# Kernel tuning notes

Measured on AMD Instinct MI355X. Metric: run time of the kernel, lower is better.

Reference implementation:

```python
import jax, jax.numpy as jnp
import numpy as np

C, S, K, SIGMA = 512, 11, 3, 16
B = 128
EPS = 1e-5  # BatchNorm eps (eval mode, running_mean=0, running_var=1)


def _make_dct_weight(Cc, H, W):
    # FcaNet 'low16' frequency selection
    lx = [0, 0, 1, 1, 0, 2, 2, 1, 2, 0, 3, 4, 0, 1, 3, 0]
    ly = [0, 1, 0, 1, 2, 0, 1, 2, 2, 3, 0, 0, 4, 3, 1, 5]
    mx = [u * (H // 7) for u in lx]
    my = [v * (W // 7) for v in ly]
    w = np.zeros((Cc, H, W), np.float32)
    cp = Cc // len(lx)

    def bf(pos, freq, POS):
        r = np.cos(np.pi * freq * (pos + 0.5) / POS) / np.sqrt(POS)
        return r if freq == 0 else r * np.sqrt(2.0)

    for i, (u, v) in enumerate(zip(mx, my)):
        for tx in range(H):
            for ty in range(W):
                w[i * cp:(i + 1) * cp, tx, ty] = bf(tx, u, H) * bf(ty, v, W)
    return jnp.asarray(w)


def _bn(f, g, b):
    # eval-mode BatchNorm2d: (f - 0)/sqrt(1+eps)*g + b, per channel (axis 1)
    s = g / jnp.sqrt(1.0 + EPS)
    return f * s[None, :, None, None] + b[None, :, None, None]


def _conv1x1(f, w, b):
    return jnp.einsum('bchw,oc->bohw', f, w) + b[None, :, None, None]


def _spatial_kernel(f, w_conv, b_conv, g_sp, b_sp):
    Bn = f.shape[0]
    s = _conv1x1(f, w_conv, b_conv)                  # (B, K*K, S, S)
    s = s.reshape(Bn, K * K, S * S).transpose(0, 2, 1)  # (B, S*S, K*K)
    s = _bn(s.reshape(Bn, S * S, K, K), g_sp, b_sp)
    return s.reshape(Bn, S * S, K * K)


def _channel_kernel(f, dct_w, fc1, fc2, g_ch, b_ch):
    y = jnp.sum(f * dct_w[None], axis=(-2, -1))      # (B, C) DCT pooling
    y = jax.nn.sigmoid(jax.nn.relu(y @ fc1.T) @ fc2.T)  # (B, C*K*K)
    y = _bn(y.reshape(-1, C, K, K), g_ch, b_ch)
    return y.reshape(-1, C, K * K)


def _unfold(f):
    # torch-style per-pixel kxk neighborhoods -> (B, C, H, W, K, K)
    p = (K + 1) // 2 - 1
    Bn, Cn, H, W = f.shape
    fp = jnp.pad(f, ((0, 0), (0, 0), (p, p), (p, p)))
    pat = jnp.stack([fp[:, :, di:di + H, dj:dj + W]
                     for di in range(K) for dj in range(K)], axis=-1)
    return pat.reshape(Bn, Cn, H, W, K, K)


def setup_inputs() -> dict:
    key = jax.random.key(0)
    ks = iter(jax.random.split(key, 32))

    def nrm(shape, s=0.02):
        return s * jax.random.normal(next(ks), shape, jnp.float32)

    def gma(shape):
        return 1.0 + 0.1 * jax.random.normal(next(ks), shape, jnp.float32)

    return dict(
        x=jax.random.normal(next(ks), (B, C, S, S), jnp.float32),
        dct_w=_make_dct_weight(C, S, S),
        w_conv=nrm((K * K, C)), b_conv=nrm((K * K,)),
        g_sp=gma((S * S,)), b_sp=nrm((S * S,), 0.05),
        g_ch=gma((C,)), b_ch=nrm((C,), 0.05),
        fc1=nrm((C // SIGMA, C)), fc2=nrm((C * K * K, C // SIGMA)),
        up_w1=nrm((2 * C, C)), up_b1=nrm((2 * C,)), up_g1=gma((2 * C,)), up_bb1=nrm((2 * C,), 0.05),
        up_w2=nrm((2 * C, 2 * C)), up_b2=nrm((2 * C,)), up_g2=gma((2 * C,)), up_bb2=nrm((2 * C,), 0.05),
        lo_w1=nrm((2 * C, 2 * C)), lo_b1=nrm((2 * C,)), lo_g1=gma((2 * C,)), lo_bb1=nrm((2 * C,), 0.05),
        lo_w2=nrm((C, 2 * C)), lo_b2=nrm((C,)), lo_g2=gma((C,)), lo_bb2=nrm((C,), 0.05),
    )


def reference(x, dct_w, w_conv, b_conv, g_sp, b_sp, g_ch, b_ch, fc1, fc2,
              up_w1, up_b1, up_g1, up_bb1, up_w2, up_b2, up_g2, up_bb2,
              lo_w1, lo_b1, lo_g1, lo_bb1, lo_w2, lo_b2, lo_g2, lo_bb2):
    Bn = x.shape[0]
    # instance kernel: spatial (B,1,HW,KK) x channel (B,C,1,KK)
    sk = _spatial_kernel(x, w_conv, b_conv, g_sp, b_sp)[:, None]
    ck = _channel_kernel(x, dct_w, fc1, fc2, g_ch, b_ch)[:, :, None]
    inst = (sk * ck).reshape(Bn, C, S, S, K, K)
    # CLM task representation (sum over batch between upper and lower)
    a = jax.nn.relu(_bn(_conv1x1(x, up_w1, up_b1), up_g1, up_bb1))
    a = jax.nn.relu(_bn(_conv1x1(a, up_w2, up_b2), up_g2, up_bb2))
    a = a.sum(axis=0, keepdims=True)
    a = jax.nn.relu(_bn(_conv1x1(a, lo_w1, lo_b1), lo_g1, lo_bb1))
    task_s = jax.nn.sigmoid(_bn(_conv1x1(a, lo_w2, lo_b2), lo_g2, lo_bb2))
    # task kernel (shared across the batch)
    sk_t = _spatial_kernel(task_s, w_conv, b_conv, g_sp, b_sp)[:, None]
    ck_t = _channel_kernel(task_s, dct_w, fc1, fc2, g_ch, b_ch)[:, :, None]
    task_kernel = (sk_t * ck_t).reshape(1, C, S, S, K, K)
    kernel = task_kernel * inst
    adapted = (_unfold(x) * kernel).mean(axis=(-1, -2))  # (B,C,S,S)
    return adapted + x, task_kernel
```

## Files before the change

kernel.cpp:

```cpp
#include <hip/hip_runtime.h>
#include <hip/hip_bf16.h>
#include <math.h>

#define BNEPS 1e-5f
#define BDIM_B 128
#define CDIM 512
#define SS 121
#define KK 9
#define MROWS (BDIM_B * SS)

typedef unsigned short u16;
typedef __bf16 bf16x8 __attribute__((ext_vector_type(8)));
typedef float f32x4 __attribute__((ext_vector_type(4)));

__device__ __forceinline__ u16 f2bf(float f) {
    union { float f; unsigned int u; } v; v.f = f;
    unsigned int r = v.u + 0x7FFF + ((v.u >> 16) & 1);
    return (u16)(r >> 16);
}
__device__ __forceinline__ float bf2f(u16 v) {
    union { unsigned int u; float f; } x; x.u = ((unsigned int)v) << 16; return x.f;
}

__device__ __forceinline__ void gld16(const u16* g, u16* l) {
    __builtin_amdgcn_global_load_lds(
        (const __attribute__((address_space(1))) void*)g,
        (__attribute__((address_space(3))) void*)l, 16, 0, 0);
}

template<int MODE>
__global__ __launch_bounds__(256)
void gemm_mfma(const u16* __restrict__ A, const u16* __restrict__ Bw,
               const float* __restrict__ bias, const float* __restrict__ g,
               const float* __restrict__ bb, void* __restrict__ out, int Kd)
{
    __shared__ __align__(16) u16 Als[128 * 32];
    __shared__ __align__(16) u16 Bls[128 * 32];

    const int tid  = threadIdx.x;
    const int lane = tid & 63;
    const int w    = tid >> 6;
    const int wm   = w >> 1, wn = w & 1;
    const int bm   = blockIdx.x * 128;
    const int bn   = blockIdx.y * 128;

    f32x4 acc[4][4] = {};

    const int subrow = tid >> 2;
    const int kq     = tid & 3;
    const u16* Ab = A  + (size_t)(bm + subrow) * Kd + kq * 8;
    const u16* Bb = Bw + (size_t)(bn + subrow) * Kd + kq * 8;
    u16* Al0 = &Als[(w * 16) * 32];
    u16* Al1 = &Als[(w * 16 + 64) * 32];
    u16* Bl0 = &Bls[(w * 16) * 32];
    u16* Bl1 = &Bls[(w * 16 + 64) * 32];

    const int fa_row = wm * 64 + (lane & 15);
    const int fb_row = wn * 64 + (lane & 15);
    const int kofs   = (lane >> 4) * 8;

    for (int k0 = 0; k0 < Kd; k0 += 32) {
        __syncthreads();
        gld16(Ab + k0, Al0);
        gld16(Ab + (size_t)64 * Kd + k0, Al1);
        gld16(Bb + k0, Bl0);
        gld16(Bb + (size_t)64 * Kd + k0, Bl1);
        __syncthreads();

        bf16x8 af[4], bfv[4];
        #pragma unroll
        for (int i = 0; i < 4; ++i)
            af[i] = *(bf16x8*)&Als[(fa_row + i * 16) * 32 + kofs];
        #pragma unroll
        for (int j = 0; j < 4; ++j)
            bfv[j] = *(bf16x8*)&Bls[(fb_row + j * 16) * 32 + kofs];
        #pragma unroll
        for (int i = 0; i < 4; ++i)
            #pragma unroll
            for (int j = 0; j < 4; ++j)
                acc[i][j] = __builtin_amdgcn_mfma_f32_16x16x32_bf16(af[i], bfv[j], acc[i][j], 0, 0, 0);
    }

    const float inv = 1.0f / sqrtf(1.0f + BNEPS);

    if (MODE == 1) {
        u16* Y = (u16*)out;
        int dstrow[4][4];
        #pragma unroll
        for (int i = 0; i < 4; ++i) {
            int mb = bm + wm * 64 + i * 16 + (lane >> 4) * 4;
            #pragma unroll
            for (int r = 0; r < 4; ++r) {
                int m = mb + r;
                int b = m / 121, p = m - b * 121;
                dstrow[i][r] = p * 128 + b;
            }
        }
        #pragma unroll
        for (int j = 0; j < 4; ++j) {
            int n = bn + wn * 64 + j * 16 + (lane & 15);
            float sc = g[n] * inv, bo = bias[n], bv = bb[n];
            #pragma unroll
            for (int i = 0; i < 4; ++i)
                #pragma unroll
                for (int r = 0; r < 4; ++r) {
                    float v = (acc[i][j][r] + bo) * sc + bv;
                    v = fmaxf(v, 0.0f);
                    Y[(size_t)dstrow[i][r] * 1024 + n] = f2bf(v);
                }
        }
    } else {
        float ps[4];
        #pragma unroll
        for (int j = 0; j < 4; ++j) {
            int n = bn + wn * 64 + j * 16 + (lane & 15);
            float sc = g[n] * inv, bo = bias[n], bv = bb[n];
            float s = 0.f;
            #pragma unroll
            for (int i = 0; i < 4; ++i)
                #pragma unroll
                for (int r = 0; r < 4; ++r) {
                    float v = (acc[i][j][r] + bo) * sc + bv;
                    s += fmaxf(v, 0.0f);
                }
            ps[j] = s;
        }
        __syncthreads();
        float* red = (float*)Als;
        #pragma unroll
        for (int j = 0; j < 4; ++j)
            red[(wm * 4 + (lane >> 4)) * 128 + wn * 64 + j * 16 + (lane & 15)] = ps[j];
        __syncthreads();
        if (tid < 128) {
            float s = 0.f;
            #pragma unroll
            for (int r = 0; r < 8; ++r) s += red[r * 128 + tid];
            ((float*)out)[(size_t)blockIdx.x * 1024 + bn + tid] = s;
        }
    }
}

__global__ void transpose_x(const float* __restrict__ x, u16* __restrict__ Xb)
{
    __shared__ float t[64 * 121];
    int b = blockIdx.x, c0 = blockIdx.y * 64;
    for (int idx = threadIdx.x; idx < 64 * 121; idx += 256) {
        int c = idx / 121, p = idx - c * 121;
        t[idx] = x[((size_t)b * 512 + c0 + c) * 121 + p];
    }
    __syncthreads();
    for (int idx = threadIdx.x; idx < 121 * 64; idx += 256) {
        int p = idx >> 6, c = idx & 63;
        Xb[((size_t)(b * 121 + p)) * 512 + c0 + c] = f2bf(t[c * 121 + p]);
    }
}

__global__ void f32_to_bf16(const float* __restrict__ in, u16* __restrict__ out, int n)
{
    int i = blockIdx.x * 256 + threadIdx.x;
    if (i < n) out[i] = f2bf(in[i]);
}

__global__ void transpose_dct(const float* __restrict__ dct, float* __restrict__ dctT)
{
    int idx = blockIdx.x * 256 + threadIdx.x;
    if (idx >= 512 * 121) return;
    int p = idx >> 9, c = idx & 511;
    dctT[idx] = dct[(size_t)c * 121 + p];
}

template<int ACT>
__global__ __launch_bounds__(256)
void fc_ksplit(const float* __restrict__ A, const float* __restrict__ W,
               const float* __restrict__ bias, const float* __restrict__ g,
               const float* __restrict__ bb, void* __restrict__ out,
               int N, int Kd)
{
    __shared__ float Als[1024];
    int p = blockIdx.x;
    const float* a = A + (size_t)p * Kd;
    for (int i = threadIdx.x; i < Kd / 4; i += 256)
        ((float4*)Als)[i] = ((const float4*)a)[i];
    __syncthreads();
    int n = blockIdx.y * 64 + (threadIdx.x >> 2);
    int kp = threadIdx.x & 3;
    const float* w = W + (size_t)n * Kd;
    float s0 = 0.f, s1 = 0.f;
    for (int k = kp * 4; k < Kd; k += 32) {
        float4 wv = *(const float4*)(w + k);
        float4 av = *(const float4*)(Als + k);
        s0 += wv.x * av.x + wv.y * av.y + wv.z * av.z + wv.w * av.w;
        float4 wv2 = *(const float4*)(w + k + 16);
        float4 av2 = *(const float4*)(Als + k + 16);
        s1 += wv2.x * av2.x + wv2.y * av2.y + wv2.z * av2.z + wv2.w * av2.w;
    }
    float s = s0 + s1;
    s += __shfl_xor(s, 1);
    s += __shfl_xor(s, 2);
    if (kp == 0) {
        s = (s + bias[n]) * (g[n] * (1.0f / sqrtf(1.0f + BNEPS))) + bb[n];
        if (ACT == 0) {
            ((float*)out)[(size_t)p * N + n] = fmaxf(s, 0.f);
        } else {
            s = 1.f / (1.f + expf(-s));
            ((u16*)out)[(size_t)p * 512 + n] = f2bf(s);
        }
    }
}

__global__ __launch_bounds__(256)
void rowdot9(const u16* __restrict__ Xb, const u16* __restrict__ Xt,
             const float* __restrict__ w_conv, const float* __restrict__ b_conv,
             const float* __restrict__ g_sp, const float* __restrict__ b_sp,
             float* __restrict__ skb, float* __restrict__ skt)
{
    int wid = (blockIdx.x * 256 + threadIdx.x) >> 6;
    int lane = threadIdx.x & 63;
    if (wid >= MROWS + SS) return;
    const u16* src = (wid < MROWS) ? Xb + (size_t)wid * 512
                                   : Xt + (size_t)(wid - MROWS) * 512;
    bf16x8 xv = *(const bf16x8*)(src + lane * 8);
    float xf[8];
    #pragma unroll
    for (int j = 0; j < 8; ++j) xf[j] = (float)xv[j];

    float s[9];
    #pragma unroll
    for (int k9 = 0; k9 < 9; ++k9) {
        const float* wr = w_conv + k9 * 512 + lane * 8;
        float4 w0 = *(const float4*)wr;
        float4 w1 = *(const float4*)(wr + 4);
        s[k9] = xf[0] * w0.x + xf[1] * w0.y + xf[2] * w0.z + xf[3] * w0.w
              + xf[4] * w1.x + xf[5] * w1.y + xf[6] * w1.z + xf[7] * w1.w;
    }
    #pragma unroll
    for (int off = 1; off < 64; off <<= 1)
        #pragma unroll
        for (int k9 = 0; k9 < 9; ++k9)
            s[k9] += __shfl_xor(s[k9], off);

    if (lane < 9) {
        int p = wid % 121;
        float v = (s[lane] + b_conv[lane]) * (g_sp[p] * (1.0f / sqrtf(1.0f + BNEPS))) + b_sp[p];
        float* dst = (wid < MROWS) ? skb + (size_t)wid * 9 : skt + (size_t)(wid - MROWS) * 9;
        dst[lane] = v;
    }
}

__global__ void dct_pool_xb(const u16* __restrict__ Xb, const u16* __restrict__ Xt,
                            const float* __restrict__ dctT,
                            float* __restrict__ ybuf, float* __restrict__ y_t)
{
    int idx = blockIdx.x * 256 + threadIdx.x;
    if (idx >= 129 * 512) return;
    int g = idx >> 9, c = idx & 511;
    const u16* src = (g < 128) ? Xb + (size_t)g * 121 * 512 + c : Xt + c;
    float s = 0.f;
    for (int p = 0; p < SS; ++p)
        s += bf2f(src[(size_t)p * 512]) * dctT[p * 512 + c];
    if (g < 128) ybuf[idx] = s; else y_t[c] = s;
}

__global__ __launch_bounds__(256)
void fc1_fused(const float* __restrict__ ybuf, const float* __restrict__ y_t,
               const float* __restrict__ fc1, float* __restrict__ y2buf,
               float* __restrict__ y2_t)
{
    __shared__ float Als[512];
    int g = blockIdx.x;
    const float* a = (g < 128) ? ybuf + (size_t)g * 512 : y_t;
    for (int i = threadIdx.x; i < 128; i += 256)
        ((float4*)Als)[i] = ((const float4*)a)[i];
    __syncthreads();
    int o = threadIdx.x >> 3, kp = threadIdx.x & 7;
    const float* w = fc1 + (size_t)o * 512;
    float s = 0.f;
    for (int k = kp * 4; k < 512; k += 32) {
        float4 wv = *(const float4*)(w + k);
        float4 av = *(const float4*)(Als + k);
        s += wv.x * av.x + wv.y * av.y + wv.z * av.z + wv.w * av.w;
    }
    s += __shfl_xor(s, 1);
    s += __shfl_xor(s, 2);
    s += __shfl_xor(s, 4);
    if (kp == 0) {
        float v = fmaxf(s, 0.f);
        if (g < 128) y2buf[(size_t)g * 32 + o] = v; else y2_t[o] = v;
    }
}

__global__ void fc2_ck_fused(const float* __restrict__ y2buf, const float* __restrict__ y2_t,
                             const float* __restrict__ fc2,
                             const float* __restrict__ g_ch, const float* __restrict__ b_ch,
                             float* __restrict__ ckbuf, float* __restrict__ ck_t)
{
    int idx = blockIdx.x * 256 + threadIdx.x;
    if (idx >= 129 * CDIM * KK) return;
    int g = idx / (CDIM * KK), o = idx % (CDIM * KK);
    int c = o / KK;
    const float* yb = (g < 128) ? y2buf + (size_t)g * 32 : y2_t;
    const float* w = fc2 + (size_t)o * 32;
    float s = 0.f;
    #pragma unroll
    for (int k = 0; k < 32; ++k) s += yb[k] * w[k];
    s = 1.f / (1.f + expf(-s));
    s = s * (g_ch[c] * (1.0f / sqrtf(1.0f + BNEPS))) + b_ch[c];
    if (g < 128) ckbuf[idx] = s; else ck_t[o] = s;
}

__global__ void task_kernel_write(const float* __restrict__ sk_t, const float* __restrict__ ck_t,
                                  float* __restrict__ tk)
{
    int idx = blockIdx.x * blockDim.x + threadIdx.x;
    if (idx >= CDIM * SS * KK) return;
    int k9 = idx % KK;
    int pc = idx / KK;
    int p = pc % SS, c = pc / SS;
    tk[idx] = sk_t[p * KK + k9] * ck_t[c * KK + k9];
}

__global__ __launch_bounds__(256)
void final_v2(const float* __restrict__ x, const float* __restrict__ skb,
              const float* __restrict__ sk_t, const float* __restrict__ ckbuf,
              const float* __restrict__ ck_t, float* __restrict__ out0)
{
    __shared__ float PS[SS * KK];
    __shared__ float CS[64 * KK];
    __shared__ float XT[64 * SS];
    const int tid = threadIdx.x;
    const int b = blockIdx.x, c0 = blockIdx.y * 64;

    const float* sp = skb + (size_t)b * SS * KK;
    for (int i = tid; i < SS * KK; i += 256) PS[i] = sp[i] * sk_t[i];
    const float* cp = ckbuf + ((size_t)b * CDIM + c0) * KK;
    const float* tp = ck_t + (size_t)c0 * KK;
    for (int i = tid; i < 64 * KK; i += 256) CS[i] = cp[i] * tp[i];
    const float* xp = x + ((size_t)b * CDIM + c0) * SS;
    for (int i = tid; i < 64 * SS; i += 256) XT[i] = xp[i];
    __syncthreads();

    float* op = out0 + ((size_t)b * CDIM + c0) * SS;
    for (int i = tid; i < 64 * SS; i += 256) {
        int c = i / SS, p = i - c * SS;
        int h = p / 11, w = p - h * 11;
        const float* xc = XT + c * SS;
        const float* ps = PS + p * KK;
        const float* cs = CS + c * KK;
        float acc = 0.f;
        #pragma unroll
        for (int di = 0; di < 3; ++di) {
            int hh = h + di - 1;
            bool hv = (unsigned)hh < 11u;
            #pragma unroll
            for (int dj = 0; dj < 3; ++dj) {
                int ww = w + dj - 1;
                int k = di * 3 + dj;
                float xv = (hv && (unsigned)ww < 11u) ? xc[hh * 11 + ww] : 0.f;
                acc += xv * ps[k] * cs[k];
            }
        }
        op[i] = acc * (1.0f / 9.0f) + xc[p];
    }
}

extern "C" void kernel_launch(void* const* d_in, const int* in_sizes, int n_in,
                              void* d_out, int out_size, void* d_ws, size_t ws_size,
                              hipStream_t stream)
{
    const float* x      = (const float*)d_in[0];
    const float* dct_w  = (const float*)d_in[1];
    const float* w_conv = (const float*)d_in[2];
    const float* b_conv = (const float*)d_in[3];
    const float* g_sp   = (const float*)d_in[4];
    const float* b_sp   = (const float*)d_in[5];
    const float* g_ch   = (const float*)d_in[6];
    const float* b_ch   = (const float*)d_in[7];
    const float* fc1    = (const float*)d_in[8];
    const float* fc2    = (const float*)d_in[9];
    const float* up_w1  = (const float*)d_in[10];
    const float* up_b1  = (const float*)d_in[11];
    const float* up_g1  = (const float*)d_in[12];
    const float* up_bb1 = (const float*)d_in[13];
    const float* up_w2  = (const float*)d_in[14];
    const float* up_b2  = (const float*)d_in[15];
    const float* up_g2  = (const float*)d_in[16];
    const float* up_bb2 = (const float*)d_in[17];
    const float* lo_w1  = (const float*)d_in[18];
    const float* lo_b1  = (const float*)d_in[19];
    const float* lo_g1  = (const float*)d_in[20];
    const float* lo_bb1 = (const float*)d_in[21];
    const float* lo_w2  = (const float*)d_in[22];
    const float* lo_b2  = (const float*)d_in[23];
    const float* lo_g2  = (const float*)d_in[24];
    const float* lo_bb2 = (const float*)d_in[25];

    float* out0 = (float*)d_out;
    float* tk   = out0 + (size_t)BDIM_B * CDIM * SS;

    char* ws = (char*)d_ws;
    size_t off = 0;
    auto alloc = [&](size_t bytes) { void* p = ws + off; off += (bytes + 63) & ~(size_t)63; return p; };
    u16*   Xb     = (u16*)alloc((size_t)MROWS * 512 * 2);
    u16*   Y1     = (u16*)alloc((size_t)MROWS * 1024 * 2);
    u16*   w1b    = (u16*)alloc((size_t)1024 * 512 * 2);
    u16*   w2b    = (u16*)alloc((size_t)1024 * 1024 * 2);
    float* asum   = (float*)alloc((size_t)SS * 1024 * 4);
    float* a3     = (float*)alloc((size_t)SS * 1024 * 4);
    u16*   ts_pc  = (u16*)alloc((size_t)SS * 512 * 2);
    float* dctT   = (float*)alloc((size_t)SS * 512 * 4);
    float* ybuf   = (float*)alloc((size_t)BDIM_B * CDIM * 4);
    float* y2buf  = (float*)alloc((size_t)BDIM_B * 32 * 4);
    float* ckbuf  = (float*)alloc((size_t)BDIM_B * CDIM * KK * 4);
    float* skbuf  = (float*)alloc((size_t)BDIM_B * SS * KK * 4);
    float* y_t    = (float*)alloc((size_t)CDIM * 4);
    float* y2_t   = (float*)alloc((size_t)32 * 4);
    float* ck_t   = (float*)alloc((size_t)CDIM * KK * 4);
    float* sk_t   = (float*)alloc((size_t)SS * KK * 4);

    hipLaunchKernelGGL(transpose_x, dim3(BDIM_B, 8), dim3(256), 0, stream, x, Xb);
    hipLaunchKernelGGL(f32_to_bf16, dim3((1024 * 512 + 255) / 256), dim3(256), 0, stream,
                       up_w1, w1b, 1024 * 512);
    hipLaunchKernelGGL(f32_to_bf16, dim3((1024 * 1024 + 255) / 256), dim3(256), 0, stream,
                       up_w2, w2b, 1024 * 1024);
    hipLaunchKernelGGL(transpose_dct, dim3((512 * 121 + 255) / 256), dim3(256), 0, stream,
                       dct_w, dctT);

    dim3 ggrid(MROWS / 128, 1024 / 128);
    hipLaunchKernelGGL((gemm_mfma<1>), ggrid, dim3(256), 0, stream,
                       Xb, w1b, up_b1, up_g1, up_bb1, (void*)Y1, 512);
    hipLaunchKernelGGL((gemm_mfma<2>), ggrid, dim3(256), 0, stream,
                       Y1, w2b, up_b2, up_g2, up_bb2, (void*)asum, 1024);

    hipLaunchKernelGGL((fc_ksplit<0>), dim3(SS, 16), dim3(256), 0, stream,
                       asum, lo_w1, lo_b1, lo_g1, lo_bb1, (void*)a3, 1024, 1024);
    hipLaunchKernelGGL((fc_ksplit<1>), dim3(SS, 8), dim3(256), 0, stream,
                       a3, lo_w2, lo_b2, lo_g2, lo_bb2, (void*)ts_pc, 512, 1024);

    hipLaunchKernelGGL(rowdot9, dim3((MROWS + SS + 3) / 4), dim3(256), 0, stream,
                       Xb, ts_pc, w_conv, b_conv, g_sp, b_sp, skbuf, sk_t);

    hipLaunchKernelGGL(dct_pool_xb, dim3((129 * 512) / 256), dim3(256), 0, stream,
                       Xb, ts_pc, dctT, ybuf, y_t);
    hipLaunchKernelGGL(fc1_fused, dim3(129), dim3(256), 0, stream,
                       ybuf, y_t, fc1, y2buf, y2_t);
    hipLaunchKernelGGL(fc2_ck_fused, dim3((129 * CDIM * KK + 255) / 256), dim3(256), 0, stream,
                       y2buf, y2_t, fc2, g_ch, b_ch, ckbuf, ck_t);

    hipLaunchKernelGGL(task_kernel_write, dim3((CDIM * SS * KK + 255) / 256), dim3(256), 0, stream,
                       sk_t, ck_t, tk);

    hipLaunchKernelGGL(final_v2, dim3(BDIM_B, 8), dim3(256), 0, stream,
                       x, skbuf, sk_t, ckbuf, ck_t, out0);
}
```

Measured before the change: 352.4 us.

## Run lower CLM layers on MFMA GEMM, swizzle LDS, merge weight conversions

New measurement: 354.3 us. No clear change (+0.5%).

```diff
diff --git a/kernel.cpp b/kernel.cpp
--- a/kernel.cpp
+++ b/kernel.cpp
@@ -32,7 +32,8 @@
 __global__ __launch_bounds__(256)
 void gemm_mfma(const u16* __restrict__ A, const u16* __restrict__ Bw,
                const float* __restrict__ bias, const float* __restrict__ g,
-               const float* __restrict__ bb, void* __restrict__ out, int Kd)
+               const float* __restrict__ bb, void* __restrict__ out,
+               int Kd, int N, int NT)
 {
     __shared__ __align__(16) u16 Als[128 * 32];
     __shared__ __align__(16) u16 Bls[128 * 32];
@@ -41,15 +42,19 @@
     const int lane = tid & 63;
     const int w    = tid >> 6;
     const int wm   = w >> 1, wn = w & 1;
-    const int bm   = blockIdx.x * 128;
-    const int bn   = blockIdx.y * 128;
+    const int lb   = blockIdx.x;
+    const int bx   = lb / NT;
+    const int by   = lb - bx * NT;
+    const int bm   = bx * 128;
+    const int bn   = by * 128;
 
     f32x4 acc[4][4] = {};
 
     const int subrow = tid >> 2;
     const int kq     = tid & 3;
-    const u16* Ab = A  + (size_t)(bm + subrow) * Kd + kq * 8;
-    const u16* Bb = Bw + (size_t)(bn + subrow) * Kd + kq * 8;
+    const int gchunk = kq ^ ((subrow >> 1) & 3);
+    const u16* Ab = A  + (size_t)(bm + subrow) * Kd + gchunk * 8;
+    const u16* Bb = Bw + (size_t)(bn + subrow) * Kd + gchunk * 8;
     u16* Al0 = &Als[(w * 16) * 32];
     u16* Al1 = &Als[(w * 16 + 64) * 32];
     u16* Bl0 = &Bls[(w * 16) * 32];
@@ -57,7 +62,7 @@
 
     const int fa_row = wm * 64 + (lane & 15);
     const int fb_row = wn * 64 + (lane & 15);
-    const int kofs   = (lane >> 4) * 8;
+    const int kofs   = (((lane >> 4) ^ (((lane & 15) >> 1) & 3))) * 8;
 
     for (int k0 = 0; k0 < Kd; k0 += 32) {
         __syncthreads();
@@ -106,10 +111,10 @@
                 for (int r = 0; r < 4; ++r) {
                     float v = (acc[i][j][r] + bo) * sc + bv;
                     v = fmaxf(v, 0.0f);
-                    Y[(size_t)dstrow[i][r] * 1024 + n] = f2bf(v);
+                    Y[(size_t)dstrow[i][r] * N + n] = f2bf(v);
                 }
         }
-    } else {
+    } else if (MODE == 2) {
         float ps[4];
         #pragma unroll
         for (int j = 0; j < 4; ++j) {
@@ -135,7 +140,25 @@
             float s = 0.f;
             #pragma unroll
             for (int r = 0; r < 8; ++r) s += red[r * 128 + tid];
-            ((float*)out)[(size_t)blockIdx.x * 1024 + bn + tid] = s;
+            ((float*)out)[(size_t)bx * N + bn + tid] = s;
+        }
+    } else {
+        u16* Y = (u16*)out;
+        #pragma unroll
+        for (int j = 0; j < 4; ++j) {
+            int n = bn + wn * 64 + j * 16 + (lane & 15);
+            float sc = g[n] * inv, bo = bias[n], bv = bb[n];
+            #pragma unroll
+            for (int i = 0; i < 4; ++i) {
+                int mb = bm + wm * 64 + i * 16 + (lane >> 4) * 4;
+                #pragma unroll
+                for (int r = 0; r < 4; ++r) {
+                    float v = (acc[i][j][r] + bo) * sc + bv;
+                    if (MODE == 3) v = fmaxf(v, 0.0f);
+                    else           v = 1.f / (1.f + expf(-v));
+                    Y[(size_t)(mb + r) * N + n] = f2bf(v);
+                }
+            }
         }
     }
 }
@@ -155,6 +178,25 @@
     }
 }
 
+#define W1N (1024 * 512)
+#define W2N (1024 * 1024)
+#define L1N (1024 * 1024)
+#define L2N (512 * 1024)
+__global__ void conv_weights(const float* __restrict__ w1, const float* __restrict__ w2,
+                             const float* __restrict__ l1, const float* __restrict__ l2,
+                             u16* __restrict__ o1, u16* __restrict__ o2,
+                             u16* __restrict__ o3, u16* __restrict__ o4)
+{
+    int i = blockIdx.x * 256 + threadIdx.x;
+    if (i < W1N) { o1[i] = f2bf(w1[i]); return; }
+    i -= W1N;
+    if (i < W2N) { o2[i] = f2bf(w2[i]); return; }
+    i -= W2N;
+    if (i < L1N) { o3[i] = f2bf(l1[i]); return; }
+    i -= L1N;
+    if (i < L2N) { o4[i] = f2bf(l2[i]); }
+}
+
 __global__ void f32_to_bf16(const float* __restrict__ in, u16* __restrict__ out, int n)
 {
     int i = blockIdx.x * 256 + threadIdx.x;
@@ -167,45 +209,6 @@
     if (idx >= 512 * 121) return;
     int p = idx >> 9, c = idx & 511;
     dctT[idx] = dct[(size_t)c * 121 + p];
-}
-
-template<int ACT>
-__global__ __launch_bounds__(256)
-void fc_ksplit(const float* __restrict__ A, const float* __restrict__ W,
-               const float* __restrict__ bias, const float* __restrict__ g,
-               const float* __restrict__ bb, void* __restrict__ out,
-               int N, int Kd)
-{
-    __shared__ float Als[1024];
-    int p = blockIdx.x;
-    const float* a = A + (size_t)p * Kd;
-    for (int i = threadIdx.x; i < Kd / 4; i += 256)
-        ((float4*)Als)[i] = ((const float4*)a)[i];
-    __syncthreads();
-    int n = blockIdx.y * 64 + (threadIdx.x >> 2);
-    int kp = threadIdx.x & 3;
-    const float* w = W + (size_t)n * Kd;
-    float s0 = 0.f, s1 = 0.f;
-    for (int k = kp * 4; k < Kd; k += 32) {
-        float4 wv = *(const float4*)(w + k);
-        float4 av = *(const float4*)(Als + k);
-        s0 += wv.x * av.x + wv.y * av.y + wv.z * av.z + wv.w * av.w;
-        float4 wv2 = *(const float4*)(w + k + 16);
-        float4 av2 = *(const float4*)(Als + k + 16);
-        s1 += wv2.x * av2.x + wv2.y * av2.y + wv2.z * av2.z + wv2.w * av2.w;
-    }
-    float s = s0 + s1;
-    s += __shfl_xor(s, 1);
-    s += __shfl_xor(s, 2);
-    if (kp == 0) {
-        s = (s + bias[n]) * (g[n] * (1.0f / sqrtf(1.0f + BNEPS))) + bb[n];
-        if (ACT == 0) {
-            ((float*)out)[(size_t)p * N + n] = fmaxf(s, 0.f);
-        } else {
-            s = 1.f / (1.f + expf(-s));
-            ((u16*)out)[(size_t)p * 512 + n] = f2bf(s);
-        }
-    }
 }
 
 __global__ __launch_bounds__(256)
@@ -400,41 +403,43 @@
     char* ws = (char*)d_ws;
     size_t off = 0;
     auto alloc = [&](size_t bytes) { void* p = ws + off; off += (bytes + 63) & ~(size_t)63; return p; };
-    u16*   Xb     = (u16*)alloc((size_t)MROWS * 512 * 2);
-    u16*   Y1     = (u16*)alloc((size_t)MROWS * 1024 * 2);
-    u16*   w1b    = (u16*)alloc((size_t)1024 * 512 * 2);
-    u16*   w2b    = (u16*)alloc((size_t)1024 * 1024 * 2);
-    float* asum   = (float*)alloc((size_t)SS * 1024 * 4);
-    float* a3     = (float*)alloc((size_t)SS * 1024 * 4);
-    u16*   ts_pc  = (u16*)alloc((size_t)SS * 512 * 2);
-    float* dctT   = (float*)alloc((size_t)SS * 512 * 4);
-    float* ybuf   = (float*)alloc((size_t)BDIM_B * CDIM * 4);
-    float* y2buf  = (float*)alloc((size_t)BDIM_B * 32 * 4);
-    float* ckbuf  = (float*)alloc((size_t)BDIM_B * CDIM * KK * 4);
-    float* skbuf  = (float*)alloc((size_t)BDIM_B * SS * KK * 4);
-    float* y_t    = (float*)alloc((size_t)CDIM * 4);
-    float* y2_t   = (float*)alloc((size_t)32 * 4);
-    float* ck_t   = (float*)alloc((size_t)CDIM * KK * 4);
-    float* sk_t   = (float*)alloc((size_t)SS * KK * 4);
+    u16*   Xb      = (u16*)alloc((size_t)MROWS * 512 * 2);
+    u16*   Y1      = (u16*)alloc((size_t)MROWS * 1024 * 2);
+    u16*   w1b     = (u16*)alloc((size_t)W1N * 2);
+    u16*   w2b     = (u16*)alloc((size_t)W2N * 2);
+    u16*   lw1b    = (u16*)alloc((size_t)L1N * 2);
+    u16*   lw2b    = (u16*)alloc((size_t)L2N * 2);
+    float* asum    = (float*)alloc((size_t)128 * 1024 * 4);
+    u16*   asum_b  = (u16*)alloc((size_t)128 * 1024 * 2);
+    u16*   a3b     = (u16*)alloc((size_t)128 * 1024 * 2);
+    u16*   ts_pc   = (u16*)alloc((size_t)128 * 512 * 2);
+    float* dctT    = (float*)alloc((size_t)SS * 512 * 4);
+    float* ybuf    = (float*)alloc((size_t)BDIM_B * CDIM * 4);
+    float* y2buf   = (float*)alloc((size_t)BDIM_B * 32 * 4);
+    float* ckbuf   = (float*)alloc((size_t)BDIM_B * CDIM * KK * 4);
+    float* skbuf   = (float*)alloc((size_t)BDIM_B * SS * KK * 4);
+    float* y_t     = (float*)alloc((size_t)CDIM * 4);
+    float* y2_t    = (float*)alloc((size_t)32 * 4);
+    float* ck_t    = (float*)alloc((size_t)CDIM * KK * 4);
+    float* sk_t    = (float*)alloc((size_t)SS * KK * 4);
 
     hipLaunchKernelGGL(transpose_x, dim3(BDIM_B, 8), dim3(256), 0, stream, x, Xb);
-    hipLaunchKernelGGL(f32_to_bf16, dim3((1024 * 512 + 255) / 256), dim3(256), 0, stream,
-                       up_w1, w1b, 1024 * 512);
-    hipLaunchKernelGGL(f32_to_bf16, dim3((1024 * 1024 + 255) / 256), dim3(256), 0, stream,
-                       up_w2, w2b, 1024 * 1024);
+    hipLaunchKernelGGL(conv_weights, dim3((W1N + W2N + L1N + L2N) / 256), dim3(256), 0, stream,
+                       up_w1, up_w2, lo_w1, lo_w2, w1b, w2b, lw1b, lw2b);
     hipLaunchKernelGGL(transpose_dct, dim3((512 * 121 + 255) / 256), dim3(256), 0, stream,
                        dct_w, dctT);
 
-    dim3 ggrid(MROWS / 128, 1024 / 128);
-    hipLaunchKernelGGL((gemm_mfma<1>), ggrid, dim3(256), 0, stream,
-                       Xb, w1b, up_b1, up_g1, up_bb1, (void*)Y1, 512);
-    hipLaunchKernelGGL((gemm_mfma<2>), ggrid, dim3(256), 0, stream,
-                       Y1, w2b, up_b2, up_g2, up_bb2, (void*)asum, 1024);
-
-    hipLaunchKernelGGL((fc_ksplit<0>), dim3(SS, 16), dim3(256), 0, stream,
-                       asum, lo_w1, lo_b1, lo_g1, lo_bb1, (void*)a3, 1024, 1024);
-    hipLaunchKernelGGL((fc_ksplit<1>), dim3(SS, 8), dim3(256), 0, stream,
-                       a3, lo_w2, lo_b2, lo_g2, lo_bb2, (void*)ts_pc, 512, 1024);
+    hipLaunchKernelGGL((gemm_mfma<1>), dim3(121 * 8), dim3(256), 0, stream,
+                       Xb, w1b, up_b1, up_g1, up_bb1, (void*)Y1, 512, 1024, 8);
+    hipLaunchKernelGGL((gemm_mfma<2>), dim3(121 * 8), dim3(256), 0, stream,
+                       Y1, w2b, up_b2, up_g2, up_bb2, (void*)asum, 1024, 1024, 8);
+
+    hipLaunchKernelGGL(f32_to_bf16, dim3((128 * 1024) / 256), dim3(256), 0, stream,
+                       asum, asum_b, 128 * 1024);
+    hipLaunchKernelGGL((gemm_mfma<3>), dim3(8), dim3(256), 0, stream,
+                       asum_b, lw1b, lo_b1, lo_g1, lo_bb1, (void*)a3b, 1024, 1024, 8);
+    hipLaunchKernelGGL((gemm_mfma<4>), dim3(4), dim3(256), 0, stream,
+                       a3b, lw2b, lo_b2, lo_g2, lo_bb2, (void*)ts_pc, 1024, 512, 4);
 
     hipLaunchKernelGGL(rowdot9, dim3((MROWS + SS + 3) / 4), dim3(256), 0, stream,
                        Xb, ts_pc, w_conv, b_conv, g_sp, b_sp, skbuf, sk_t);
```
